# Performance work log

Measured on AMD Instinct MI355X. Metric: run time of the kernel, lower is better.

## Reference

```python
import jax, jax.numpy as jnp
import numpy as np

N = 50000          # nodes
E = 800000         # edges (before self-loops)
F_IN, F_HID, F_OUT = 128, 64, 64
NEG_SLOPE_ATT = 0.2   # GATConv internal leaky_relu
NEG_SLOPE_ACT = 0.01  # F.leaky_relu default between layers


def setup_inputs() -> dict:
    key = jax.random.key(0)
    ks = jax.random.split(key, 16)

    def glorot(k, shape):
        fan = float(sum(shape)) if len(shape) > 1 else float(shape[0])
        return jax.random.normal(k, shape, jnp.float32) * (2.0 / fan) ** 0.5

    return {
        "x": jax.random.normal(ks[0], (N, F_IN), jnp.float32),
        "edge_index": jax.random.randint(ks[1], (2, E), 0, N, dtype=jnp.int64),
        "W1": glorot(ks[2], (F_IN, F_HID)),
        "a_src1": glorot(ks[3], (F_HID,)),
        "a_dst1": glorot(ks[4], (F_HID,)),
        "b1": jnp.zeros((F_HID,), jnp.float32),
        "W2": glorot(ks[5], (F_HID, F_HID)),
        "a_src2": glorot(ks[6], (F_HID,)),
        "a_dst2": glorot(ks[7], (F_HID,)),
        "b2": jnp.zeros((F_HID,), jnp.float32),
        "W3": glorot(ks[8], (F_HID, F_OUT)),
        "a_src3": glorot(ks[9], (F_OUT,)),
        "a_dst3": glorot(ks[10], (F_OUT,)),
        "b3": jnp.zeros((F_OUT,), jnp.float32),
    }


def gat_conv(h, src, dst, W, a_src, a_dst, b):
    # Single-head PyG GATConv: project, per-edge scores, segment softmax over dst, scatter-add.
    z = h @ W                              # [N, C]
    e_src = z @ a_src                      # [N]
    e_dst = z @ a_dst                      # [N]
    e = jax.nn.leaky_relu(e_src[src] + e_dst[dst], NEG_SLOPE_ATT)  # [E']
    m = jax.ops.segment_max(e, dst, num_segments=N)
    ex = jnp.exp(e - m[dst])
    denom = jax.ops.segment_sum(ex, dst, num_segments=N)
    alpha = ex / (denom[dst] + 1e-16)      # segment softmax (PyG adds 1e-16)
    out = jax.ops.segment_sum(alpha[:, None] * z[src], dst, num_segments=N) + b
    return out, alpha


def reference(x, edge_index, W1, a_src1, a_dst1, b1, W2, a_src2, a_dst2, b2, W3, a_src3, a_dst3, b3):
    # add_self_loops=True (GATConv default): append (i, i) for every node
    loops = jnp.arange(N, dtype=edge_index.dtype)
    ei = jnp.concatenate([edge_index, jnp.stack([loops, loops])], axis=1)  # [2, E+N]
    src, dst = ei[0], ei[1]

    h = x
    alpha = None
    for (W, asr, ads, b) in ((W1, a_src1, a_dst1, b1),
                             (W2, a_src2, a_dst2, b2),
                             (W3, a_src3, a_dst3, b3)):
        h, alpha = gat_conv(h, src, dst, W, asr, ads, b)
        h = jax.nn.leaky_relu(h, NEG_SLOPE_ACT)
    return (h, ei, alpha)
```

## Files before the change

kernel.cpp:

```cpp
#include <hip/hip_runtime.h>
#include <hip/hip_bf16.h>
#include <hip/hip_fp8.h>

#define NN 50000
#define EE 800000
#define E2 850000
#define F_IN 128
#define F_HID 64
#define NCHUNK ((NN + 255) / 256)
#define NTILE  ((NN + 63) / 64)
#define AGGB 2048

#define PNB 32
#define BCAP 32768
#define HBCH 1024
#define HBB ((EE + HBCH - 1) / HBCH)
#define HCAP 64
#define SLICEB 64
#define BSPAN 1563

__device__ __forceinline__ unsigned char f32_to_fp8(float x) {
    __hip_fp8_e4m3 t(x);
    return t.__x;
}
__device__ __forceinline__ float fp8_to_f32(unsigned char b) {
    __hip_fp8_e4m3 t; t.__x = b;
    return (float)t;
}

#if defined(__has_builtin)
#  if __has_builtin(__builtin_amdgcn_cvt_f32_fp8)
#    define CVT_FP8(v, s) __builtin_amdgcn_cvt_f32_fp8((v), (s))
#  endif
#endif
#ifndef CVT_FP8
#  define CVT_FP8(v, s) fp8_to_f32(((v) >> (8 * (s))) & 255)
#endif

__global__ __launch_bounds__(256) void cast_bin(const int* __restrict__ ei,
                                                int* __restrict__ bin_cur,
                                                unsigned long long* __restrict__ bins,
                                                float* __restrict__ ei_out) {
    __shared__ unsigned long long buf[PNB * HCAP];
    __shared__ int wcnt[4][PNB];
    __shared__ int woff[4][PNB];
    __shared__ int tcn[PNB];
    __shared__ int gbase[PNB];
    __shared__ int pfx[PNB + 1];

    int tid = threadIdx.x, lane = tid & 63, wv = tid >> 6;
    if (tid < 4 * PNB) ((int*)wcnt)[tid] = 0;
    __syncthreads();

    int e0 = blockIdx.x * HBCH;
    int nE = EE - e0; if (nE > HBCH) nE = HBCH;

    int sR[4], dR[4], bR[4], rk[4];
    bool act[4];
#pragma unroll
    for (int it = 0; it < 4; ++it) {
        int idx = it * 256 + tid;
        bool a = idx < nE;
        act[it] = a;
        int e = e0 + idx;
        int ss = 0, dd = 0;
        if (a) { ss = ei[e]; dd = ei[EE + e]; }
        if (a) {
            ei_out[e]      = (float)ss;
            ei_out[E2 + e] = (float)dd;
        }
        int bb = a ? (int)(((long long)dd * PNB) / NN) : -1;
        int myrank = 0;
        for (int bin = 0; bin < PNB; ++bin) {
            unsigned long long m = __ballot(bb == bin);
            if (bb == bin) {
                int base = wcnt[wv][bin];
                int lr = __popcll(m & ((1ull << lane) - 1));
                myrank = base + lr;
                if (lr == 0) wcnt[wv][bin] = base + __popcll(m);
            }
        }
        sR[it] = ss; dR[it] = dd; bR[it] = bb; rk[it] = myrank;
    }
    __syncthreads();

    if (tid < PNB) {
        int b = tid, r = 0;
        for (int w2 = 0; w2 < 4; ++w2) { int c = wcnt[w2][b]; woff[w2][b] = r; r += c; }
        int cl = (r > HCAP) ? HCAP : r;
        tcn[b] = cl;
        gbase[b] = cl ? atomicAdd(&bin_cur[b], cl) : 0;
    }
    __syncthreads();
    if (tid == 0) {
        int run = 0;
        for (int b = 0; b < PNB; ++b) { pfx[b] = run; run += tcn[b]; }
        pfx[PNB] = run;
    }
    __syncthreads();

#pragma unroll
    for (int it = 0; it < 4; ++it) {
        if (act[it]) {
            int b = bR[it];
            int idx = woff[wv][b] + rk[it];
            unsigned long long pk =
                ((unsigned long long)(unsigned)dR[it] << 32) | (unsigned)sR[it];
            if (idx < HCAP) buf[b * HCAP + idx] = pk;
            else {
                int p = atomicAdd(&bin_cur[b], 1);
                if (p < BCAP) bins[(size_t)b * BCAP + p] = pk;
            }
        }
    }
    __syncthreads();

    int total = pfx[PNB];
    for (int idx = tid; idx < total; idx += 256) {
        int lo = 0, hi = PNB;
        while (hi - lo > 1) { int mid = (lo + hi) >> 1; if (pfx[mid] <= idx) lo = mid; else hi = mid; }
        int b = lo, li = idx - pfx[b];
        int p = gbase[b] + li;
        if (p < BCAP) bins[(size_t)b * BCAP + p] = buf[b * HCAP + li];
    }
}

__global__ __launch_bounds__(1024) void count_lds(const int* __restrict__ bin_cur,
                                                  const unsigned long long* __restrict__ bins,
                                                  int* __restrict__ deg) {
    __shared__ int cnt[BSPAN];
    int b = blockIdx.x;
    int lo = (int)(((long long)b * NN + PNB - 1) / PNB);
    int hi = (int)(((long long)(b + 1) * NN + PNB - 1) / PNB);
    int span = hi - lo;
    for (int i = threadIdx.x; i < span; i += 1024) cnt[i] = 0;
    __syncthreads();
    int n = bin_cur[b]; if (n > BCAP) n = BCAP;
    const unsigned long long* bp = bins + (size_t)b * BCAP;
    for (int i = threadIdx.x; i < n; i += 1024) {
        int d = (int)(bp[i] >> 32);
        atomicAdd(&cnt[d - lo], 1);
    }
    __syncthreads();
    for (int i = threadIdx.x; i < span; i += 1024) deg[lo + i] = cnt[i];
}

__global__ __launch_bounds__(256) void scan_part12(const int* __restrict__ deg,
                                                   int* __restrict__ csum,
                                                   int* __restrict__ ticket) {
    int i = blockIdx.x * 256 + threadIdx.x;
    int v = (i < NN) ? deg[i] + 1 : 0;
#pragma unroll
    for (int d = 32; d; d >>= 1) v += __shfl_xor(v, d);
    __shared__ int ws[4];
    if ((threadIdx.x & 63) == 0) ws[threadIdx.x >> 6] = v;
    __syncthreads();
    __shared__ int isLast;
    if (threadIdx.x == 0) {
        atomicExch(&csum[blockIdx.x], ws[0] + ws[1] + ws[2] + ws[3]);
        __threadfence();
        isLast = (atomicAdd(ticket, 1) == gridDim.x - 1) ? 1 : 0;
    }
    __syncthreads();
    if (isLast) {
        __threadfence();
        __shared__ int sd[256];
        int t = threadIdx.x;
        int v2 = (t < NCHUNK) ? atomicAdd(&csum[t], 0) : 0;
        sd[t] = v2;
        __syncthreads();
        for (int off = 1; off < 256; off <<= 1) {
            int o = (t >= off) ? sd[t - off] : 0;
            __syncthreads();
            sd[t] += o;
            __syncthreads();
        }
        if (t < NCHUNK) atomicExch(&csum[t], sd[t] - v2);
    }
}

__global__ __launch_bounds__(256) void scan_part3(const int* __restrict__ deg,
                                                  const int* __restrict__ csum,
                                                  int* __restrict__ offs,
                                                  int* __restrict__ cursor,
                                                  int* __restrict__ src_sorted,
                                                  float* __restrict__ ei_out) {
    __shared__ int sd[256];
    int t = threadIdx.x;
    int i = blockIdx.x * 256 + t;
    int v = (i < NN) ? deg[i] + 1 : 0;
    sd[t] = v;
    __syncthreads();
    for (int off = 1; off < 256; off <<= 1) {
        int o = (t >= off) ? sd[t - off] : 0;
        __syncthreads();
        sd[t] += o;
        __syncthreads();
    }
    if (i < NN) {
        int ex = sd[t] - v + csum[blockIdx.x];
        offs[i] = ex;
        cursor[i] = ex + 1;
        src_sorted[ex] = i;
        ei_out[EE + i]      = (float)i;
        ei_out[E2 + EE + i] = (float)i;
    }
}

__global__ __launch_bounds__(256) void scatter_bins(const int* __restrict__ bin_cur,
                                                    const unsigned long long* __restrict__ bins,
                                                    int* __restrict__ cursor,
                                                    int* __restrict__ src_sorted) {
    int b = blockIdx.x & (PNB - 1);
    int slice = blockIdx.x >> 5;
    int cnt = bin_cur[b];
    if (cnt > BCAP) cnt = BCAP;
    const unsigned long long* bp = bins + (size_t)b * BCAP;
    for (int i = slice * 256 + threadIdx.x; i < cnt; i += SLICEB * 256) {
        unsigned long long v = bp[i];
        int d = (int)(v >> 32);
        int s = (int)(v & 0xffffffffu);
        int pos = atomicAdd(&cursor[d], 1);
        src_sorted[pos] = s;
    }
}

template <int K>
__global__ __launch_bounds__(256) void gemm_tile(const float* __restrict__ h,
                                                 const float* __restrict__ W,
                                                 const float* __restrict__ a_src,
                                                 const float* __restrict__ a_dst,
                                                 unsigned char* __restrict__ z8,
                                                 float* __restrict__ es,
                                                 float* __restrict__ ed) {
    constexpr int LDA = K + 4;
    __shared__ float Alds[64 * LDA];
    __shared__ float Blds[K * 64];

    int tid = threadIdx.x;
    int base = blockIdx.x * 64;

    {
        constexpr int F4R = K / 4;
        for (int t = tid; t < 64 * F4R; t += 256) {
            int r = t / F4R;
            int c4 = t % F4R;
            int gr = base + r;
            if (gr >= NN) gr = NN - 1;
            float4 v = *(const float4*)(h + (size_t)gr * K + c4 * 4);
            *(float4*)(&Alds[r * LDA + c4 * 4]) = v;
        }
    }
    for (int t = tid; t < K * 16; t += 256) {
        float4 v = *(const float4*)(W + t * 4);
        *(float4*)(&Blds[t * 4]) = v;
    }
    __syncthreads();

    int tx = tid & 15;
    int ty = tid >> 4;

    float acc[4][4] = {};
#pragma unroll 4
    for (int k = 0; k < K; k += 4) {
        float4 a[4], b[4];
#pragma unroll
        for (int i = 0; i < 4; ++i)
            a[i] = *(const float4*)(&Alds[(4 * ty + i) * LDA + k]);
#pragma unroll
        for (int kk = 0; kk < 4; ++kk)
            b[kk] = *(const float4*)(&Blds[(k + kk) * 64 + 4 * tx]);
#pragma unroll
        for (int i = 0; i < 4; ++i) {
            acc[i][0] = fmaf(a[i].x, b[0].x, acc[i][0]);
            acc[i][1] = fmaf(a[i].x, b[0].y, acc[i][1]);
            acc[i][2] = fmaf(a[i].x, b[0].z, acc[i][2]);
            acc[i][3] = fmaf(a[i].x, b[0].w, acc[i][3]);
            acc[i][0] = fmaf(a[i].y, b[1].x, acc[i][0]);
            acc[i][1] = fmaf(a[i].y, b[1].y, acc[i][1]);
            acc[i][2] = fmaf(a[i].y, b[1].z, acc[i][2]);
            acc[i][3] = fmaf(a[i].y, b[1].w, acc[i][3]);
            acc[i][0] = fmaf(a[i].z, b[2].x, acc[i][0]);
            acc[i][1] = fmaf(a[i].z, b[2].y, acc[i][1]);
            acc[i][2] = fmaf(a[i].z, b[2].z, acc[i][2]);
            acc[i][3] = fmaf(a[i].z, b[2].w, acc[i][3]);
            acc[i][0] = fmaf(a[i].w, b[3].x, acc[i][0]);
            acc[i][1] = fmaf(a[i].w, b[3].y, acc[i][1]);
            acc[i][2] = fmaf(a[i].w, b[3].z, acc[i][2]);
            acc[i][3] = fmaf(a[i].w, b[3].w, acc[i][3]);
        }
    }

    float4 as4 = *(const float4*)(a_src + 4 * tx);
    float4 ad4 = *(const float4*)(a_dst + 4 * tx);
    float ps[4], pd[4];
#pragma unroll
    for (int i = 0; i < 4; ++i) {
        int gr = base + 4 * ty + i;
        if (gr < NN) {
            unsigned int pk = (unsigned int)f32_to_fp8(acc[i][0])
                            | ((unsigned int)f32_to_fp8(acc[i][1]) << 8)
                            | ((unsigned int)f32_to_fp8(acc[i][2]) << 16)
                            | ((unsigned int)f32_to_fp8(acc[i][3]) << 24);
            *(unsigned int*)(&z8[(size_t)gr * 64 + 4 * tx]) = pk;
        }
        ps[i] = acc[i][0] * as4.x + acc[i][1] * as4.y + acc[i][2] * as4.z + acc[i][3] * as4.w;
        pd[i] = acc[i][0] * ad4.x + acc[i][1] * ad4.y + acc[i][2] * ad4.z + acc[i][3] * ad4.w;
    }
#pragma unroll
    for (int d = 1; d < 16; d <<= 1) {
#pragma unroll
        for (int i = 0; i < 4; ++i) {
            ps[i] += __shfl_xor(ps[i], d);
            pd[i] += __shfl_xor(pd[i], d);
        }
    }
    if (tx == 0) {
#pragma unroll
        for (int i = 0; i < 4; ++i) {
            int gr = base + 4 * ty + i;
            if (gr < NN) { es[gr] = ps[i]; ed[gr] = pd[i]; }
        }
    }
}

__global__ __launch_bounds__(256) void aggregate(const int* __restrict__ offs,
                                                 const int* __restrict__ deg,
                                                 const int* __restrict__ src_sorted,
                                                 const float* __restrict__ es,
                                                 const float* __restrict__ ed,
                                                 const unsigned char* __restrict__ z8,
                                                 const float* __restrict__ bias,
                                                 float* __restrict__ hout,
                                                 float* __restrict__ denom_out) {
    __shared__ unsigned long long swl[4][64];
    int tid = threadIdx.x;
    int lane = tid & 63;
    int wslot = tid >> 6;
    int wave = blockIdx.x * 4 + wslot;
    const int NW = AGGB * 4;

    int sub  = lane >> 4;
    int fgrp = (lane & 15) * 4;
    const unsigned char* zp = z8 + fgrp;
    float4 bi4 = *(const float4*)(bias + fgrp);

    int n = wave;
    if (n >= NN) return;
    n = __builtin_amdgcn_readfirstlane(n);
    int off = offs[n];
    int dg = deg[n] + 1;
    float edn = ed[n];
    int sv = src_sorted[off + ((lane < dg) ? lane : 0)];
    float ese = es[sv];

    while (true) {
        int n2 = n + NW;
        bool more = (n2 < NN);
        int off2 = 0, dg2 = 0; float edn2 = 0.f;
        if (more) {
            n2 = __builtin_amdgcn_readfirstlane(n2);
            off2 = offs[n2]; dg2 = deg[n2] + 1; edn2 = ed[n2];
        }

        float dsum = 0.f;
        float a0 = 0.f, a1 = 0.f, a2 = 0.f, a3 = 0.f;
        for (int b0 = 0; b0 < dg; b0 += 64) {
            int bl = dg - b0; if (bl > 64) bl = 64;
            int svb; float esv;
            if (b0 == 0) { svb = sv; esv = ese; }
            else {
                svb = src_sorted[off + b0 + ((lane < bl) ? lane : 0)];
                esv = es[svb];
            }
            float e = esv + edn;
            e = (e > 0.f) ? e : 0.2f * e;
            float w = (lane < bl) ? __expf(e) : 0.f;
            dsum += w;

            swl[wslot][lane] = ((unsigned long long)__float_as_uint(w) << 32)
                             | (unsigned)(svb << 6);

            int ng = (bl + 3) >> 2;
            int j = 0;
            for (; j + 4 <= ng; j += 4) {
                int i0 = 4 * j + sub;
                unsigned long long p0 = swl[wslot][i0];
                unsigned long long p1 = swl[wslot][i0 + 4];
                unsigned long long p2 = swl[wslot][i0 + 8];
                unsigned long long p3 = swl[wslot][i0 + 12];
                unsigned int v0 = *(const unsigned int*)(zp + (unsigned)p0);
                unsigned int v1 = *(const unsigned int*)(zp + (unsigned)p1);
                unsigned int v2 = *(const unsigned int*)(zp + (unsigned)p2);
                unsigned int v3 = *(const unsigned int*)(zp + (unsigned)p3);
                float w0 = __uint_as_float((unsigned)(p0 >> 32));
                float w1 = __uint_as_float((unsigned)(p1 >> 32));
                float w2 = __uint_as_float((unsigned)(p2 >> 32));
                float w3 = __uint_as_float((unsigned)(p3 >> 32));
                a0 = fmaf(w0, CVT_FP8(v0, 0), a0);
                a1 = fmaf(w0, CVT_FP8(v0, 1), a1);
                a2 = fmaf(w0, CVT_FP8(v0, 2), a2);
                a3 = fmaf(w0, CVT_FP8(v0, 3), a3);
                a0 = fmaf(w1, CVT_FP8(v1, 0), a0);
                a1 = fmaf(w1, CVT_FP8(v1, 1), a1);
                a2 = fmaf(w1, CVT_FP8(v1, 2), a2);
                a3 = fmaf(w1, CVT_FP8(v1, 3), a3);
                a0 = fmaf(w2, CVT_FP8(v2, 0), a0);
                a1 = fmaf(w2, CVT_FP8(v2, 1), a1);
                a2 = fmaf(w2, CVT_FP8(v2, 2), a2);
                a3 = fmaf(w2, CVT_FP8(v2, 3), a3);
                a0 = fmaf(w3, CVT_FP8(v3, 0), a0);
                a1 = fmaf(w3, CVT_FP8(v3, 1), a1);
                a2 = fmaf(w3, CVT_FP8(v3, 2), a2);
                a3 = fmaf(w3, CVT_FP8(v3, 3), a3);
            }
            for (; j < ng; ++j) {
                int i0 = 4 * j + sub;
                unsigned long long p0 = swl[wslot][i0];
                unsigned int v0 = *(const unsigned int*)(zp + (unsigned)p0);
                float w0 = __uint_as_float((unsigned)(p0 >> 32));
                a0 = fmaf(w0, CVT_FP8(v0, 0), a0);
                a1 = fmaf(w0, CVT_FP8(v0, 1), a1);
                a2 = fmaf(w0, CVT_FP8(v0, 2), a2);
                a3 = fmaf(w0, CVT_FP8(v0, 3), a3);
            }
        }

        int sv2 = 0;
        if (more) sv2 = src_sorted[off2 + ((lane < dg2) ? lane : 0)];

        a0 += __shfl_xor(a0, 16); a1 += __shfl_xor(a1, 16);
        a2 += __shfl_xor(a2, 16); a3 += __shfl_xor(a3, 16);
        a0 += __shfl_xor(a0, 32); a1 += __shfl_xor(a1, 32);
        a2 += __shfl_xor(a2, 32); a3 += __shfl_xor(a3, 32);
#pragma unroll
        for (int d = 32; d; d >>= 1) dsum += __shfl_xor(dsum, d);

        float ese2 = 0.f;
        if (more) ese2 = es[sv2];

        float inv = 1.f / (dsum + 1e-16f);
        if (lane < 16) {
            float4 o;
            o.x = a0 * inv + bi4.x;
            o.y = a1 * inv + bi4.y;
            o.z = a2 * inv + bi4.z;
            o.w = a3 * inv + bi4.w;
            o.x = (o.x > 0.f) ? o.x : 0.01f * o.x;
            o.y = (o.y > 0.f) ? o.y : 0.01f * o.y;
            o.z = (o.z > 0.f) ? o.z : 0.01f * o.z;
            o.w = (o.w > 0.f) ? o.w : 0.01f * o.w;
            *(float4*)(hout + (size_t)n * 64 + fgrp) = o;
        }
        if (lane == 0) denom_out[n] = dsum;

        if (!more) break;
        n = n2; off = off2; dg = dg2; edn = edn2; sv = sv2; ese = ese2;
    }
}

__global__ __launch_bounds__(256) void alpha_kernel(const int* __restrict__ ei,
                                                    const float* __restrict__ es,
                                                    const float* __restrict__ ed,
                                                    const float* __restrict__ denom,
                                                    float* __restrict__ alpha_out) {
    int e = blockIdx.x * 256 + threadIdx.x;
    if (e >= E2) return;
    int s, d;
    if (e < EE) { s = ei[e]; d = ei[EE + e]; }
    else        { s = d = e - EE; }
    float x = es[s] + ed[d];
    x = (x > 0.f) ? x : 0.2f * x;
    alpha_out[e] = __expf(x) / (denom[d] + 1e-16f);
}

extern "C" void kernel_launch(void* const* d_in, const int* in_sizes, int n_in,
                              void* d_out, int out_size, void* d_ws, size_t ws_size,
                              hipStream_t stream) {
    const float* x   = (const float*)d_in[0];
    const int*   ei  = (const int*)d_in[1];
    const float* W1  = (const float*)d_in[2];
    const float* as1 = (const float*)d_in[3];
    const float* ad1 = (const float*)d_in[4];
    const float* b1  = (const float*)d_in[5];
    const float* W2  = (const float*)d_in[6];
    const float* as2 = (const float*)d_in[7];
    const float* ad2 = (const float*)d_in[8];
    const float* b2  = (const float*)d_in[9];
    const float* W3  = (const float*)d_in[10];
    const float* as3 = (const float*)d_in[11];
    const float* ad3 = (const float*)d_in[12];
    const float* b3  = (const float*)d_in[13];

    float* out       = (float*)d_out;
    float* h_out     = out;
    float* ei_out    = out + (size_t)NN * 64;
    float* alpha_out = ei_out + 2 * (size_t)E2;

    char* w = (char*)d_ws;
    auto carve = [&](size_t bytes) {
        void* p = (void*)w;
        w += (bytes + 255) & ~size_t(255);
        return p;
    };
    float* h1  = (float*)carve((size_t)NN * 64 * 4);
    float* h2  = (float*)carve((size_t)NN * 64 * 4);
    unsigned char* z8 = (unsigned char*)carve((size_t)NN * 64);
    float* es  = (float*)carve((size_t)NN * 4);
    float* ed  = (float*)carve((size_t)NN * 4);
    float* denom = (float*)carve((size_t)NN * 4);
    int* deg        = (int*)carve(((size_t)NN + 64) * 4);
    int* ticket     = deg + NN;
    int* bin_cur    = deg + NN + 1;
    int* offs       = (int*)carve((size_t)NN * 4);
    int* cursor     = (int*)carve((size_t)NN * 4);
    int* csum       = (int*)carve((size_t)NCHUNK * 4);
    int* src_sorted = (int*)carve((size_t)E2 * 4);
    unsigned long long* bins = (unsigned long long*)carve((size_t)PNB * BCAP * 8);

    const int EB = (E2 + 255) / 256;

    hipMemsetAsync(deg + NN, 0, 64 * 4, stream);
    cast_bin<<<HBB, 256, 0, stream>>>(ei, bin_cur, bins, ei_out);
    count_lds<<<PNB, 1024, 0, stream>>>(bin_cur, bins, deg);
    scan_part12<<<NCHUNK, 256, 0, stream>>>(deg, csum, ticket);
    scan_part3<<<NCHUNK, 256, 0, stream>>>(deg, csum, offs, cursor, src_sorted, ei_out);
    scatter_bins<<<PNB * SLICEB, 256, 0, stream>>>(bin_cur, bins, cursor, src_sorted);

    gemm_tile<F_IN><<<NTILE, 256, 0, stream>>>(x, W1, as1, ad1, z8, es, ed);
    aggregate<<<AGGB, 256, 0, stream>>>(offs, deg, src_sorted, es, ed, z8, b1, h1, denom);
    gemm_tile<F_HID><<<NTILE, 256, 0, stream>>>(h1, W2, as2, ad2, z8, es, ed);
    aggregate<<<AGGB, 256, 0, stream>>>(offs, deg, src_sorted, es, ed, z8, b2, h2, denom);
    gemm_tile<F_HID><<<NTILE, 256, 0, stream>>>(h2, W3, as3, ad3, z8, es, ed);
    aggregate<<<AGGB, 256, 0, stream>>>(offs, deg, src_sorted, es, ed, z8, b3, h_out, denom);
    alpha_kernel<<<EB, 256, 0, stream>>>(ei, es, ed, denom, alpha_out);
}
```

Before: 291.8 us.

## Fuse degree count and prefix scan into one kernel with inter-block spin barrier

```diff
diff --git a/kernel.cpp b/kernel.cpp
--- a/kernel.cpp
+++ b/kernel.cpp
@@ -7,15 +7,14 @@
 #define E2 850000
 #define F_IN 128
 #define F_HID 64
-#define NCHUNK ((NN + 255) / 256)
 #define NTILE  ((NN + 63) / 64)
 #define AGGB 2048
 
 #define PNB 32
 #define BCAP 32768
-#define HBCH 1024
-#define HBB ((EE + HBCH - 1) / HBCH)
-#define HCAP 64
+#define HBCH 512
+#define CBB2 ((EE + HBCH - 1) / HBCH)
+#define HCAP 40
 #define SLICEB 64
 #define BSPAN 1563
 
@@ -48,39 +47,30 @@
     __shared__ int gbase[PNB];
     __shared__ int pfx[PNB + 1];
 
-    int tid = threadIdx.x, lane = tid & 63, wv = tid >> 6;
+    int tid = threadIdx.x, wv = tid >> 6;
     if (tid < 4 * PNB) ((int*)wcnt)[tid] = 0;
     __syncthreads();
 
     int e0 = blockIdx.x * HBCH;
     int nE = EE - e0; if (nE > HBCH) nE = HBCH;
 
-    int sR[4], dR[4], bR[4], rk[4];
-    bool act[4];
-#pragma unroll
-    for (int it = 0; it < 4; ++it) {
+    int sR[2], dR[2], bR[2], rk[2];
+    bool act[2];
+#pragma unroll
+    for (int it = 0; it < 2; ++it) {
         int idx = it * 256 + tid;
         bool a = idx < nE;
         act[it] = a;
         int e = e0 + idx;
-        int ss = 0, dd = 0;
-        if (a) { ss = ei[e]; dd = ei[EE + e]; }
+        int ss = 0, dd = 0, bb = 0, r = 0;
         if (a) {
+            ss = ei[e]; dd = ei[EE + e];
             ei_out[e]      = (float)ss;
             ei_out[E2 + e] = (float)dd;
-        }
-        int bb = a ? (int)(((long long)dd * PNB) / NN) : -1;
-        int myrank = 0;
-        for (int bin = 0; bin < PNB; ++bin) {
-            unsigned long long m = __ballot(bb == bin);
-            if (bb == bin) {
-                int base = wcnt[wv][bin];
-                int lr = __popcll(m & ((1ull << lane) - 1));
-                myrank = base + lr;
-                if (lr == 0) wcnt[wv][bin] = base + __popcll(m);
-            }
-        }
-        sR[it] = ss; dR[it] = dd; bR[it] = bb; rk[it] = myrank;
+            bb = (int)(((long long)dd * PNB) / NN);
+            r = atomicAdd(&wcnt[wv][bb], 1);
+        }
+        sR[it] = ss; dR[it] = dd; bR[it] = bb; rk[it] = r;
     }
     __syncthreads();
 
@@ -100,7 +90,7 @@
     __syncthreads();
 
 #pragma unroll
-    for (int it = 0; it < 4; ++it) {
+    for (int it = 0; it < 2; ++it) {
         if (act[it]) {
             int b = bR[it];
             int idx = woff[wv][b] + rk[it];
@@ -125,85 +115,98 @@
     }
 }
 
-__global__ __launch_bounds__(1024) void count_lds(const int* __restrict__ bin_cur,
-                                                  const unsigned long long* __restrict__ bins,
-                                                  int* __restrict__ deg) {
+__global__ __launch_bounds__(1024) void count_scan(const int* __restrict__ bin_cur,
+                                                   const unsigned long long* __restrict__ bins,
+                                                   int* __restrict__ deg,
+                                                   int* __restrict__ offs,
+                                                   int* __restrict__ cursor,
+                                                   int* __restrict__ src_sorted,
+                                                   float* __restrict__ ei_out,
+                                                   int* __restrict__ ticket,
+                                                   int* __restrict__ flag,
+                                                   int* __restrict__ bsum,
+                                                   int* __restrict__ bbase) {
     __shared__ int cnt[BSPAN];
+    __shared__ int wsm[16];
+    __shared__ int totsh, lastsh, basesh;
+    int t = threadIdx.x, lane = t & 63, wid = t >> 6;
     int b = blockIdx.x;
     int lo = (int)(((long long)b * NN + PNB - 1) / PNB);
     int hi = (int)(((long long)(b + 1) * NN + PNB - 1) / PNB);
+    if (hi > NN) hi = NN;
     int span = hi - lo;
-    for (int i = threadIdx.x; i < span; i += 1024) cnt[i] = 0;
+    for (int i = t; i < span; i += 1024) cnt[i] = 0;
     __syncthreads();
     int n = bin_cur[b]; if (n > BCAP) n = BCAP;
     const unsigned long long* bp = bins + (size_t)b * BCAP;
-    for (int i = threadIdx.x; i < n; i += 1024) {
-        int d = (int)(bp[i] >> 32);
-        atomicAdd(&cnt[d - lo], 1);
-    }
-    __syncthreads();
-    for (int i = threadIdx.x; i < span; i += 1024) deg[lo + i] = cnt[i];
-}
-
-__global__ __launch_bounds__(256) void scan_part12(const int* __restrict__ deg,
-                                                   int* __restrict__ csum,
-                                                   int* __restrict__ ticket) {
-    int i = blockIdx.x * 256 + threadIdx.x;
-    int v = (i < NN) ? deg[i] + 1 : 0;
-#pragma unroll
-    for (int d = 32; d; d >>= 1) v += __shfl_xor(v, d);
-    __shared__ int ws[4];
-    if ((threadIdx.x & 63) == 0) ws[threadIdx.x >> 6] = v;
-    __syncthreads();
-    __shared__ int isLast;
-    if (threadIdx.x == 0) {
-        atomicExch(&csum[blockIdx.x], ws[0] + ws[1] + ws[2] + ws[3]);
+    for (int i = t; i < n; i += 1024)
+        atomicAdd(&cnt[(int)(bp[i] >> 32) - lo], 1);
+    __syncthreads();
+
+    int i0 = 2 * t, i1 = 2 * t + 1;
+    int v0 = (i0 < span) ? cnt[i0] + 1 : 0;
+    int v1 = (i1 < span) ? cnt[i1] + 1 : 0;
+    int s = v0 + v1, inc = s;
+#pragma unroll
+    for (int dd = 1; dd < 64; dd <<= 1) {
+        int o = __shfl_up(inc, dd);
+        if (lane >= dd) inc += o;
+    }
+    if (lane == 63) wsm[wid] = inc;
+    __syncthreads();
+    if (t < 16) {
+        int v = wsm[t], ii = v;
+#pragma unroll
+        for (int dd = 1; dd < 16; dd <<= 1) {
+            int o = __shfl_up(ii, dd);
+            if (t >= dd) ii += o;
+        }
+        wsm[t] = ii - v;
+        if (t == 15) totsh = ii;
+    }
+    __syncthreads();
+    int eth = wsm[wid] + (inc - s);
+
+    if (t == 0) {
+        atomicExch(&bsum[b], totsh);
         __threadfence();
-        isLast = (atomicAdd(ticket, 1) == gridDim.x - 1) ? 1 : 0;
-    }
-    __syncthreads();
-    if (isLast) {
-        __threadfence();
-        __shared__ int sd[256];
-        int t = threadIdx.x;
-        int v2 = (t < NCHUNK) ? atomicAdd(&csum[t], 0) : 0;
-        sd[t] = v2;
-        __syncthreads();
-        for (int off = 1; off < 256; off <<= 1) {
-            int o = (t >= off) ? sd[t - off] : 0;
-            __syncthreads();
-            sd[t] += o;
-            __syncthreads();
-        }
-        if (t < NCHUNK) atomicExch(&csum[t], sd[t] - v2);
-    }
-}
-
-__global__ __launch_bounds__(256) void scan_part3(const int* __restrict__ deg,
-                                                  const int* __restrict__ csum,
-                                                  int* __restrict__ offs,
-                                                  int* __restrict__ cursor,
-                                                  int* __restrict__ src_sorted,
-                                                  float* __restrict__ ei_out) {
-    __shared__ int sd[256];
-    int t = threadIdx.x;
-    int i = blockIdx.x * 256 + t;
-    int v = (i < NN) ? deg[i] + 1 : 0;
-    sd[t] = v;
-    __syncthreads();
-    for (int off = 1; off < 256; off <<= 1) {
-        int o = (t >= off) ? sd[t - off] : 0;
-        __syncthreads();
-        sd[t] += o;
-        __syncthreads();
-    }
-    if (i < NN) {
-        int ex = sd[t] - v + csum[blockIdx.x];
-        offs[i] = ex;
-        cursor[i] = ex + 1;
-        src_sorted[ex] = i;
-        ei_out[EE + i]      = (float)i;
-        ei_out[E2 + EE + i] = (float)i;
+        lastsh = (atomicAdd(ticket, 1) == PNB - 1) ? 1 : 0;
+    }
+    __syncthreads();
+    if (lastsh) {
+        if (t == 0) {
+            int run = 0;
+            for (int q = 0; q < PNB; ++q) {
+                int v = atomicAdd(&bsum[q], 0);
+                atomicExch(&bbase[q], run);
+                run += v;
+            }
+            __threadfence();
+            atomicExch(flag, 1);
+        }
+    } else {
+        if (t == 0) {
+            while (atomicAdd(flag, 0) == 0) __builtin_amdgcn_s_sleep(8);
+        }
+    }
+    __syncthreads();
+    if (t == 0) basesh = atomicAdd(&bbase[b], 0);
+    __syncthreads();
+    int base = basesh;
+
+    if (i0 < span) {
+        int d = lo + i0, ex = base + eth;
+        offs[d] = ex; cursor[d] = ex + 1; deg[d] = v0 - 1;
+        src_sorted[ex] = d;
+        ei_out[EE + d]      = (float)d;
+        ei_out[E2 + EE + d] = (float)d;
+    }
+    if (i1 < span) {
+        int d = lo + i1, ex = base + eth + v0;
+        offs[d] = ex; cursor[d] = ex + 1; deg[d] = v1 - 1;
+        src_sorted[ex] = d;
+        ei_out[EE + d]      = (float)d;
+        ei_out[E2 + EE + d] = (float)d;
     }
 }
 
@@ -509,22 +512,23 @@
     float* es  = (float*)carve((size_t)NN * 4);
     float* ed  = (float*)carve((size_t)NN * 4);
     float* denom = (float*)carve((size_t)NN * 4);
-    int* deg        = (int*)carve(((size_t)NN + 64) * 4);
+    int* deg        = (int*)carve(((size_t)NN + 160) * 4);
     int* ticket     = deg + NN;
-    int* bin_cur    = deg + NN + 1;
+    int* flag       = deg + NN + 1;
+    int* bin_cur    = deg + NN + 2;
+    int* bsum       = deg + NN + 34;
+    int* bbase      = deg + NN + 66;
     int* offs       = (int*)carve((size_t)NN * 4);
     int* cursor     = (int*)carve((size_t)NN * 4);
-    int* csum       = (int*)carve((size_t)NCHUNK * 4);
     int* src_sorted = (int*)carve((size_t)E2 * 4);
     unsigned long long* bins = (unsigned long long*)carve((size_t)PNB * BCAP * 8);
 
     const int EB = (E2 + 255) / 256;
 
-    hipMemsetAsync(deg + NN, 0, 64 * 4, stream);
-    cast_bin<<<HBB, 256, 0, stream>>>(ei, bin_cur, bins, ei_out);
-    count_lds<<<PNB, 1024, 0, stream>>>(bin_cur, bins, deg);
-    scan_part12<<<NCHUNK, 256, 0, stream>>>(deg, csum, ticket);
-    scan_part3<<<NCHUNK, 256, 0, stream>>>(deg, csum, offs, cursor, src_sorted, ei_out);
+    hipMemsetAsync(deg + NN, 0, 160 * 4, stream);
+    cast_bin<<<CBB2, 256, 0, stream>>>(ei, bin_cur, bins, ei_out);
+    count_scan<<<PNB, 1024, 0, stream>>>(bin_cur, bins, deg, offs, cursor,
+                                         src_sorted, ei_out, ticket, flag, bsum, bbase);
     scatter_bins<<<PNB * SLICEB, 256, 0, stream>>>(bin_cur, bins, cursor, src_sorted);
 
     gemm_tile<F_IN><<<NTILE, 256, 0, stream>>>(x, W1, as1, ad1, z8, es, ed);
```

Measured after the change: 290.0 us, median of 2. Within noise of the previous version (-0.6%).
